# Kernel optimization log

Measured on AMD Instinct MI355X. Metric: run time of the kernel, lower is better.

## Reference

```python
import jax, jax.numpy as jnp
import numpy as np
import math

IN_DIM = 512
OUT_DIM = 512
KEY_DIM = 512
N_HEADS = 8
HEAD_DIM = KEY_DIM // N_HEADS
B, S = 2, 2048


def setup_inputs() -> dict:
    key = jax.random.key(0)
    ks = jax.random.split(key, 9)
    sc = 0.02
    return {
        "x": jax.random.normal(ks[0], (B, IN_DIM, S), dtype=jnp.float32),
        "wq": jax.random.normal(ks[1], (KEY_DIM, IN_DIM), dtype=jnp.float32) * sc,
        "bq": jax.random.normal(ks[2], (KEY_DIM,), dtype=jnp.float32) * sc,
        "wk": jax.random.normal(ks[3], (KEY_DIM, IN_DIM), dtype=jnp.float32) * sc,
        "bk": jax.random.normal(ks[4], (KEY_DIM,), dtype=jnp.float32) * sc,
        "wv": jax.random.normal(ks[5], (OUT_DIM, IN_DIM), dtype=jnp.float32) * sc,
        "bv": jax.random.normal(ks[6], (OUT_DIM,), dtype=jnp.float32) * sc,
        "wo": jax.random.normal(ks[7], (OUT_DIM, OUT_DIM), dtype=jnp.float32) * sc,
        "bo": jax.random.normal(ks[8], (OUT_DIM,), dtype=jnp.float32) * sc,
    }


def reference(x, wq, bq, wk, bk, wv, bv, wo, bo):
    # x: (B, C, S). Conv1d with kernel_size=1 == channelwise linear.
    b, _, s = x.shape
    vd = OUT_DIM // N_HEADS  # per-head value dim
    # projections: (B, key_dim, S) -> (B, H, hd, S)
    q = (jnp.einsum('oc,bcs->bos', wq, x) + bq[None, :, None]).reshape(b, N_HEADS, HEAD_DIM, s)
    k = (jnp.einsum('oc,bcs->bos', wk, x) + bk[None, :, None]).reshape(b, N_HEADS, HEAD_DIM, s)
    v = (jnp.einsum('oc,bcs->bos', wv, x) + bv[None, :, None]).reshape(b, N_HEADS, vd, s)
    # scores: (B, H, S, S) = q^T k / sqrt(hd)
    scores = jnp.einsum('bhdt,bhds->bhts', q, k) / math.sqrt(HEAD_DIM)
    attn = jax.nn.softmax(scores, axis=-1)
    # out: (B, H, S_query, vd) -> (B, out_dim, S)
    out = jnp.einsum('bhts,bhds->bhtd', attn, v)
    out = out.transpose(0, 1, 3, 2).reshape(b, OUT_DIM, s)
    out = jnp.einsum('oc,bcs->bos', wo, out) + bo[None, :, None]
    return out
```

## Files before the change

kernel.cpp:

```cpp
#include <hip/hip_runtime.h>
#include <hip/hip_bf16.h>


typedef __attribute__((ext_vector_type(8))) short short8;
typedef __attribute__((ext_vector_type(4))) short short4v;
typedef __attribute__((ext_vector_type(4))) float f32x4;
typedef __attribute__((ext_vector_type(2))) int int2v;

#define DEV static __device__ __forceinline__

DEV short f2bf(float f) {
  union { float f; unsigned u; } v; v.f = f;
  unsigned r = (v.u + 0x7FFFu + ((v.u >> 16) & 1u)) >> 16;
  return (short)r;
}

DEV float bf2f(short s) {
  union { unsigned u; float f; } v;
  v.u = ((unsigned)(unsigned short)s) << 16;
  return v.f;
}

DEV unsigned pk_bf16(float lo, float hi) {
  union { __hip_bfloat162 h; unsigned u; } cv;
  cv.h = __float22bfloat162_rn(float2{lo, hi});
  return cv.u;
}

DEV void gload_lds16(const void* g, void* l) {
  __builtin_amdgcn_global_load_lds((const __attribute__((address_space(1))) void*)g,
                                   (__attribute__((address_space(3))) void*)l, 16, 0, 0);
}

__global__ __launch_bounds__(256) void xpose_k(const float* __restrict__ x, short* __restrict__ xt) {
  __shared__ float tile[32][33];
  const int b = blockIdx.z;
  const int s0 = blockIdx.x * 32, c0 = blockIdx.y * 32;
  const int tl = threadIdx.x & 31, tr = threadIdx.x >> 5;
  const float* src = x + ((size_t)b * 512 + c0) * 2048 + s0;
#pragma unroll
  for (int i = 0; i < 4; ++i)
    tile[tr + i * 8][tl] = src[(size_t)(tr + i * 8) * 2048 + tl];
  __syncthreads();
  short* dst = xt + ((size_t)b * 2048 + s0) * 512 + c0;
#pragma unroll
  for (int i = 0; i < 4; ++i) {
    const int s = tr + i * 8;
    dst[(size_t)s * 512 + tl] = f2bf(tile[tl][s]);
  }
}

__global__ __launch_bounds__(256) void wconv_k(const float* __restrict__ wq, const float* __restrict__ wk,
                                               const float* __restrict__ wv, const float* __restrict__ wo,
                                               short* __restrict__ dst) {
  const int idx = blockIdx.x * 256 + threadIdx.x;
  const int m = idx >> 16;
  const int base = (idx & 65535) * 4;
  const float* src = (m == 0) ? wq : (m == 1) ? wk : (m == 2) ? wv : wo;
  const f32x4 v = *(const f32x4*)(src + base);
  short4v o;
#pragma unroll
  for (int r = 0; r < 4; ++r) o[r] = f2bf(v[r]);
  *(short4v*)(dst + (size_t)idx * 4) = o;
}

template <int MODE>
__global__ __launch_bounds__(256) void gemm_bt_k(const short* __restrict__ A, const short* __restrict__ B,
                                                 void* __restrict__ out, short* __restrict__ out2,
                                                 const float* __restrict__ bias0,
                                                 const float* __restrict__ bias1,
                                                 const float* __restrict__ bias2) {
  constexpr int TM = (MODE == 0) ? 128 : 64;
  constexpr int MI = TM / 32;
  constexpr int ABLK = TM / 32;
  constexpr int NI = (MODE == 0) ? 12 : 64;
  constexpr int CHUNK = (MODE == 0) ? 48 : 32;
  __shared__ short As[TM * 64];
  __shared__ short Bs[128 * 64];
  const int bx0 = blockIdx.x;
  const int bx = (bx0 & 7) * CHUNK + (bx0 >> 3);
  const int it = bx % NI, jt = bx / NI;
  const int tid = threadIdx.x;
  const int lane = tid & 63, wid = tid >> 6;
  const int wi = wid & 1, wj = wid >> 1;
  const int g = lane >> 4, c = lane & 15;

  f32x4 acc[MI][4] = {};

  for (int k0 = 0; k0 < 512; k0 += 64) {
#pragma unroll
    for (int q = 0; q < ABLK; ++q) {
      const int blk = wid * ABLK + q;
      const int row = blk * 8 + (lane >> 3);
      const int ks = ((lane & 7) ^ (row & 7)) * 8;
      gload_lds16(A + (size_t)(it * TM + row) * 512 + k0 + ks, As + blk * 512);
    }
#pragma unroll
    for (int q = 0; q < 4; ++q) {
      const int blk = wid * 4 + q;
      const int row = blk * 8 + (lane >> 3);
      const int ks = ((lane & 7) ^ (row & 7)) * 8;
      gload_lds16(B + (size_t)(jt * 128 + row) * 512 + k0 + ks, Bs + blk * 512);
    }
    __syncthreads();
#pragma unroll
    for (int kk = 0; kk < 2; ++kk) {
      short8 af[MI], bfv[4];
#pragma unroll
      for (int mi = 0; mi < MI; ++mi) {
        const int row = wi * (TM / 2) + mi * 16 + c;
        af[mi] = *(const short8*)(As + ((row * 64 + kk * 32 + g * 8) ^ ((row & 7) << 3)));
      }
#pragma unroll
      for (int nj = 0; nj < 4; ++nj) {
        const int row = wj * 64 + nj * 16 + c;
        bfv[nj] = *(const short8*)(Bs + ((row * 64 + kk * 32 + g * 8) ^ ((row & 7) << 3)));
      }
#pragma unroll
      for (int mi = 0; mi < MI; ++mi)
#pragma unroll
        for (int nj = 0; nj < 4; ++nj)
          acc[mi][nj] = __builtin_amdgcn_mfma_f32_16x16x32_bf16(af[mi], bfv[nj], acc[mi][nj], 0, 0, 0);
    }
    __syncthreads();
  }

  if constexpr (MODE == 0) {
    short* ob = (short*)out;
#pragma unroll
    for (int mi = 0; mi < MI; ++mi) {
      const int i0 = it * 128 + wi * 64 + mi * 16 + g * 4;
      if (i0 < 1024) {
        const bool isQ = i0 < 512;
        const float scale = isQ ? 0.125f : 1.0f;
        const float* bp = isQ ? bias0 : bias1;
        const int boff = isQ ? 0 : 512;
        float b4[4];
#pragma unroll
        for (int r = 0; r < 4; ++r) b4[r] = bp[i0 + r - boff];
#pragma unroll
        for (int nj = 0; nj < 4; ++nj) {
          const int j = jt * 128 + wj * 64 + nj * 16 + c;
          short4v st;
#pragma unroll
          for (int r = 0; r < 4; ++r) st[r] = f2bf((acc[mi][nj][r] + b4[r]) * scale);
          *(short4v*)(ob + (size_t)j * 1024 + i0) = st;
        }
      } else {
        float b4[4];
#pragma unroll
        for (int r = 0; r < 4; ++r) b4[r] = bias2[i0 + r - 1024];
#pragma unroll
        for (int nj = 0; nj < 4; ++nj) {
          const int j = jt * 128 + wj * 64 + nj * 16 + c;
#pragma unroll
          for (int r = 0; r < 4; ++r)
            out2[(size_t)(i0 + r - 1024) * 4096 + j] = f2bf(acc[mi][nj][r] + b4[r]);
        }
      }
    }
  } else {
    float* ob = (float*)out;
#pragma unroll
    for (int mi = 0; mi < MI; ++mi) {
      const int i0 = it * 64 + wi * 32 + mi * 16 + g * 4;
      const int bb = i0 >> 11, t = i0 & 2047;
#pragma unroll
      for (int nj = 0; nj < 4; ++nj) {
        const int j = jt * 128 + wj * 64 + nj * 16 + c;
        const float bj = bias0[j];
        f32x4 st;
#pragma unroll
        for (int r = 0; r < 4; ++r) st[r] = acc[mi][nj][r] + bj;
        *(f32x4*)(ob + ((size_t)(bb * 512 + j)) * 2048 + t) = st;
      }
    }
  }
}

__global__ __launch_bounds__(256, 4) void attn_k(const short* __restrict__ qk, const short* __restrict__ v,
                                                 short* __restrict__ OPB, float* __restrict__ Lb) {
  __shared__ short ks2[2][64 * 64];
  __shared__ short vs2[2][64 * 64];
  __shared__ short pbuf[4][32 * 64];
  const int bid = blockIdx.x;
  const int swz = (bid & 7) * 128 + (bid >> 3);
  const int qt = swz & 15;
  const int grp = swz >> 4;
  const int bh = grp & 15, seg = grp >> 4;
  const int b = bh >> 3, h = bh & 7;
  const int lane = threadIdx.x & 63, wid = threadIdx.x >> 6;
  const int g = lane >> 4, c = lane & 15;
  const int q0 = qt * 128 + wid * 32;
  short* pl = pbuf[wid];

  const short* qp = qk + (size_t)(b * 2048 + q0) * 1024 + h * 64;
  const short* kb = qk + (size_t)(b * 2048) * 1024 + 512 + h * 64;
  const short* vb = v + (size_t)(h * 64) * 4096 + b * 2048;

  short8 qf[2][2];
#pragma unroll
  for (int nj = 0; nj < 2; ++nj)
#pragma unroll
    for (int kk = 0; kk < 2; ++kk)
      qf[nj][kk] = *(const short8*)(qp + (size_t)(nj * 16 + c) * 1024 + kk * 32 + g * 8);

  const int sr = lane >> 3;
  const int scol = ((lane & 7) ^ sr) * 8;

  const int kvbeg = seg * 512;
#pragma unroll
  for (int q = 0; q < 2; ++q) {
    const int blk = wid * 2 + q;
    const int row = blk * 8 + sr;
    gload_lds16(kb + (size_t)(kvbeg + row) * 1024 + scol, &ks2[0][blk * 512]);
    gload_lds16(vb + (size_t)row * 4096 + kvbeg + scol, &vs2[0][blk * 512]);
  }

  f32x4 oacc[4][2] = {};
  float lpart[2] = {0.f, 0.f};
  const float LOG2E = 1.44269504088896f;
  const float M2 = 5.770780163555852f;

  for (int it8 = 0; it8 < 8; ++it8) {
    const int bufi = it8 & 1;

    {
      const int kvn = kvbeg + ((it8 + 1) & 7) * 64;
#pragma unroll
      for (int q = 0; q < 2; ++q) {
        const int blk = wid * 2 + q;
        const int row = blk * 8 + sr;
        gload_lds16(kb + (size_t)(kvn + row) * 1024 + scol, &ks2[bufi ^ 1][blk * 512]);
        gload_lds16(vb + (size_t)row * 4096 + kvn + scol, &vs2[bufi ^ 1][blk * 512]);
      }
    }

    asm volatile("s_waitcnt vmcnt(4)" ::: "memory");
    __builtin_amdgcn_s_barrier();

    f32x4 st[4][2] = {};
    __builtin_amdgcn_s_setprio(1);
#pragma unroll
    for (int kk = 0; kk < 2; ++kk) {
      short8 kf[4];
#pragma unroll
      for (int mi = 0; mi < 4; ++mi) {
        const int row = mi * 16 + c;
        kf[mi] = *(const short8*)(&ks2[bufi][(row * 64 + kk * 32 + g * 8) ^ ((row & 7) << 3)]);
      }
#pragma unroll
      for (int mi = 0; mi < 4; ++mi)
#pragma unroll
        for (int nj = 0; nj < 2; ++nj)
          st[mi][nj] = __builtin_amdgcn_mfma_f32_16x16x32_bf16(kf[mi], qf[nj][kk], st[mi][nj], 0, 0, 0);
    }
    __builtin_amdgcn_s_setprio(0);

#pragma unroll
    for (int mi = 0; mi < 4; ++mi)
#pragma unroll
      for (int nj = 0; nj < 2; ++nj) {
        const float p0 = __builtin_amdgcn_exp2f(__builtin_fmaf(st[mi][nj][0], LOG2E, -M2));
        const float p1 = __builtin_amdgcn_exp2f(__builtin_fmaf(st[mi][nj][1], LOG2E, -M2));
        const float p2 = __builtin_amdgcn_exp2f(__builtin_fmaf(st[mi][nj][2], LOG2E, -M2));
        const float p3 = __builtin_amdgcn_exp2f(__builtin_fmaf(st[mi][nj][3], LOG2E, -M2));
        lpart[nj] += (p0 + p1) + (p2 + p3);
        const unsigned w0 = pk_bf16(p0, p1);
        const unsigned w1 = pk_bf16(p2, p3);
        const int t = nj * 16 + c;
        *(int2v*)(pl + ((t * 64 + mi * 16 + g * 4) ^ ((t & 7) << 3))) = (int2v){(int)w0, (int)w1};
      }

    __builtin_amdgcn_s_setprio(1);
#pragma unroll
    for (int kk = 0; kk < 2; ++kk) {
      short8 vf[4], pa[2];
#pragma unroll
      for (int dj = 0; dj < 4; ++dj) {
        const int row = dj * 16 + c;
        vf[dj] = *(const short8*)(&vs2[bufi][(row * 64 + kk * 32 + g * 8) ^ ((row & 7) << 3)]);
      }
#pragma unroll
      for (int o = 0; o < 2; ++o) {
        const int row = o * 16 + c;
        pa[o] = *(const short8*)(pl + ((row * 64 + kk * 32 + g * 8) ^ ((row & 7) << 3)));
      }
#pragma unroll
      for (int dj = 0; dj < 4; ++dj)
#pragma unroll
        for (int o = 0; o < 2; ++o)
          oacc[dj][o] = __builtin_amdgcn_mfma_f32_16x16x32_bf16(vf[dj], pa[o], oacc[dj][o], 0, 0, 0);
    }
    __builtin_amdgcn_s_setprio(0);

    asm volatile("s_waitcnt lgkmcnt(0)" ::: "memory");
    __builtin_amdgcn_s_barrier();
  }

  float lrow[2];
#pragma unroll
  for (int nj = 0; nj < 2; ++nj) {
    float a = lpart[nj];
    a += __shfl_xor(a, 16);
    a += __shfl_xor(a, 32);
    lrow[nj] = a;
  }
  const size_t rbase = (size_t)seg * 32768 + (size_t)bh * 2048 + q0;
#pragma unroll
  for (int o = 0; o < 2; ++o) {
    const int t = o * 16 + c;
#pragma unroll
    for (int dj = 0; dj < 4; ++dj) {
      short4v w;
#pragma unroll
      for (int r = 0; r < 4; ++r) w[r] = f2bf(oacc[dj][o][r]);
      *(short4v*)(OPB + (rbase + t) * 64 + dj * 16 + g * 4) = w;
    }
    if (g == 0) Lb[rbase + t] = lrow[o];
  }
  asm volatile("s_waitcnt vmcnt(0)" ::: "memory");
}

__global__ __launch_bounds__(256) void merge_k(const short* __restrict__ OPB, const float* __restrict__ Lb,
                                               short* __restrict__ o) {
  const int gid = blockIdx.x * 256 + threadIdx.x;
  const int row = gid >> 2;
  const int dg = (gid & 3) * 16;
  float L = 0.f;
#pragma unroll
  for (int s = 0; s < 4; ++s) L += Lb[s * 32768 + row];
  const float rinv = 1.f / L;
  float acc[16];
#pragma unroll
  for (int j = 0; j < 16; ++j) acc[j] = 0.f;
#pragma unroll
  for (int s = 0; s < 4; ++s) {
#pragma unroll
    for (int q = 0; q < 2; ++q) {
      const short8 vv = *(const short8*)(OPB + ((size_t)s * 32768 + row) * 64 + dg + q * 8);
#pragma unroll
      for (int r = 0; r < 8; ++r) acc[q * 8 + r] += bf2f(vv[r]);
    }
  }
  const int bh = row >> 11, srow = row & 2047;
  const int b = bh >> 3, h = bh & 7;
  short8 st[2];
#pragma unroll
  for (int j = 0; j < 16; ++j) st[j >> 3][j & 7] = f2bf(acc[j] * rinv);
  short* dst = o + (size_t)(b * 2048 + srow) * 512 + h * 64 + dg;
  *(short8*)dst = st[0];
  *(short8*)(dst + 8) = st[1];
}

extern "C" void kernel_launch(void* const* d_in, const int* in_sizes, int n_in,
                              void* d_out, int out_size, void* d_ws, size_t ws_size,
                              hipStream_t stream) {
  const float* x  = (const float*)d_in[0];
  const float* wq = (const float*)d_in[1];
  const float* bq = (const float*)d_in[2];
  const float* wk = (const float*)d_in[3];
  const float* bk = (const float*)d_in[4];
  const float* wv = (const float*)d_in[5];
  const float* bv = (const float*)d_in[6];
  const float* wo = (const float*)d_in[7];
  const float* bo = (const float*)d_in[8];

  short* XT  = (short*)d_ws;
  short* WQKV = XT + (size_t)4096 * 512;
  short* WO  = WQKV + (size_t)1536 * 512;
  short* QKB = WO + (size_t)512 * 512;
  short* VB  = QKB + (size_t)4096 * 1024;
  short* OB  = VB + (size_t)512 * 4096;
  short* OPB = OB + (size_t)4096 * 512;
  float* Lb  = (float*)(OPB + (size_t)4 * 32768 * 64);

  xpose_k<<<dim3(64, 16, 2), 256, 0, stream>>>(x, XT);
  wconv_k<<<dim3(1024), 256, 0, stream>>>(wq, wk, wv, wo, WQKV);
  gemm_bt_k<0><<<dim3(384), 256, 0, stream>>>(WQKV, XT, (void*)QKB, VB, bq, bk, bv);
  attn_k<<<dim3(1024), 256, 0, stream>>>(QKB, VB, OPB, Lb);
  merge_k<<<dim3(512), 256, 0, stream>>>(OPB, Lb, OB);
  gemm_bt_k<2><<<dim3(256), 256, 0, stream>>>(OB, WO, d_out, nullptr, bo, nullptr, nullptr);
}
```

Baseline: 75.45 us.

## Fuse split-KV merge into output projection GEMM and merge prep kernels

Folds the split-KV merge (summing four partial outputs and normalising by the summed row sums) into the A-tile load of the output projection GEMM, so the normalised attention output is written straight to shared memory instead of round-tripping through a global buffer. It also combines the transpose and weight-conversion kernels into one launch and specialises the GEMM template to its QKV mode. In the attention loop it moves the barrier to the top of each iteration with a full vmcnt(0) wait before issuing the next prefetch, dropping the end-of-iteration lgkm wait and barrier. This removes two launches and an intermediate buffer, but the output GEMM now redoes the merge work once per column tile (four times in total), and the attention loop's prefetch overlap changes.

```diff
diff --git a/kernel.cpp b/kernel.cpp
--- a/kernel.cpp
+++ b/kernel.cpp
@@ -6,6 +6,7 @@
 typedef __attribute__((ext_vector_type(4))) short short4v;
 typedef __attribute__((ext_vector_type(4))) float f32x4;
 typedef __attribute__((ext_vector_type(2))) int int2v;
+typedef __attribute__((ext_vector_type(4))) int int4v;
 
 #define DEV static __device__ __forceinline__
 
@@ -32,36 +33,38 @@
                                    (__attribute__((address_space(3))) void*)l, 16, 0, 0);
 }
 
-__global__ __launch_bounds__(256) void xpose_k(const float* __restrict__ x, short* __restrict__ xt) {
+__global__ __launch_bounds__(256) void prep_k(const float* __restrict__ x, short* __restrict__ xt,
+                                              const float* __restrict__ wq, const float* __restrict__ wk,
+                                              const float* __restrict__ wv, const float* __restrict__ wo,
+                                              short* __restrict__ wdst) {
   __shared__ float tile[32][33];
-  const int b = blockIdx.z;
-  const int s0 = blockIdx.x * 32, c0 = blockIdx.y * 32;
-  const int tl = threadIdx.x & 31, tr = threadIdx.x >> 5;
-  const float* src = x + ((size_t)b * 512 + c0) * 2048 + s0;
-#pragma unroll
-  for (int i = 0; i < 4; ++i)
-    tile[tr + i * 8][tl] = src[(size_t)(tr + i * 8) * 2048 + tl];
-  __syncthreads();
-  short* dst = xt + ((size_t)b * 2048 + s0) * 512 + c0;
-#pragma unroll
-  for (int i = 0; i < 4; ++i) {
-    const int s = tr + i * 8;
-    dst[(size_t)s * 512 + tl] = f2bf(tile[tl][s]);
-  }
-}
-
-__global__ __launch_bounds__(256) void wconv_k(const float* __restrict__ wq, const float* __restrict__ wk,
-                                               const float* __restrict__ wv, const float* __restrict__ wo,
-                                               short* __restrict__ dst) {
-  const int idx = blockIdx.x * 256 + threadIdx.x;
-  const int m = idx >> 16;
-  const int base = (idx & 65535) * 4;
-  const float* src = (m == 0) ? wq : (m == 1) ? wk : (m == 2) ? wv : wo;
-  const f32x4 v = *(const f32x4*)(src + base);
-  short4v o;
-#pragma unroll
-  for (int r = 0; r < 4; ++r) o[r] = f2bf(v[r]);
-  *(short4v*)(dst + (size_t)idx * 4) = o;
+  const int bid = blockIdx.x;
+  if (bid < 2048) {
+    const int b = bid >> 10, rest = bid & 1023;
+    const int s0 = (rest & 63) * 32, c0 = (rest >> 6) * 32;
+    const int tl = threadIdx.x & 31, tr = threadIdx.x >> 5;
+    const float* src = x + ((size_t)b * 512 + c0) * 2048 + s0;
+#pragma unroll
+    for (int i = 0; i < 4; ++i)
+      tile[tr + i * 8][tl] = src[(size_t)(tr + i * 8) * 2048 + tl];
+    __syncthreads();
+    short* dst = xt + ((size_t)b * 2048 + s0) * 512 + c0;
+#pragma unroll
+    for (int i = 0; i < 4; ++i) {
+      const int s = tr + i * 8;
+      dst[(size_t)s * 512 + tl] = f2bf(tile[tl][s]);
+    }
+  } else {
+    const int idx = (bid - 2048) * 256 + threadIdx.x;
+    const int m = idx >> 16;
+    const int base = (idx & 65535) * 4;
+    const float* src = (m == 0) ? wq : (m == 1) ? wk : (m == 2) ? wv : wo;
+    const f32x4 v = *(const f32x4*)(src + base);
+    short4v o;
+#pragma unroll
+    for (int r = 0; r < 4; ++r) o[r] = f2bf(v[r]);
+    *(short4v*)(wdst + (size_t)idx * 4) = o;
+  }
 }
 
 template <int MODE>
@@ -70,12 +73,9 @@
                                                  const float* __restrict__ bias0,
                                                  const float* __restrict__ bias1,
                                                  const float* __restrict__ bias2) {
-  constexpr int TM = (MODE == 0) ? 128 : 64;
-  constexpr int MI = TM / 32;
-  constexpr int ABLK = TM / 32;
-  constexpr int NI = (MODE == 0) ? 12 : 64;
-  constexpr int CHUNK = (MODE == 0) ? 48 : 32;
-  __shared__ short As[TM * 64];
+  constexpr int NI = 12;
+  constexpr int CHUNK = 48;
+  __shared__ short As[128 * 64];
   __shared__ short Bs[128 * 64];
   const int bx0 = blockIdx.x;
   const int bx = (bx0 & 7) * CHUNK + (bx0 >> 3);
@@ -85,30 +85,24 @@
   const int wi = wid & 1, wj = wid >> 1;
   const int g = lane >> 4, c = lane & 15;
 
-  f32x4 acc[MI][4] = {};
+  f32x4 acc[4][4] = {};
 
   for (int k0 = 0; k0 < 512; k0 += 64) {
-#pragma unroll
-    for (int q = 0; q < ABLK; ++q) {
-      const int blk = wid * ABLK + q;
-      const int row = blk * 8 + (lane >> 3);
-      const int ks = ((lane & 7) ^ (row & 7)) * 8;
-      gload_lds16(A + (size_t)(it * TM + row) * 512 + k0 + ks, As + blk * 512);
-    }
 #pragma unroll
     for (int q = 0; q < 4; ++q) {
       const int blk = wid * 4 + q;
       const int row = blk * 8 + (lane >> 3);
       const int ks = ((lane & 7) ^ (row & 7)) * 8;
+      gload_lds16(A + (size_t)(it * 128 + row) * 512 + k0 + ks, As + blk * 512);
       gload_lds16(B + (size_t)(jt * 128 + row) * 512 + k0 + ks, Bs + blk * 512);
     }
     __syncthreads();
 #pragma unroll
     for (int kk = 0; kk < 2; ++kk) {
-      short8 af[MI], bfv[4];
-#pragma unroll
-      for (int mi = 0; mi < MI; ++mi) {
-        const int row = wi * (TM / 2) + mi * 16 + c;
+      short8 af[4], bfv[4];
+#pragma unroll
+      for (int mi = 0; mi < 4; ++mi) {
+        const int row = wi * 64 + mi * 16 + c;
         af[mi] = *(const short8*)(As + ((row * 64 + kk * 32 + g * 8) ^ ((row & 7) << 3)));
       }
 #pragma unroll
@@ -117,7 +111,7 @@
         bfv[nj] = *(const short8*)(Bs + ((row * 64 + kk * 32 + g * 8) ^ ((row & 7) << 3)));
       }
 #pragma unroll
-      for (int mi = 0; mi < MI; ++mi)
+      for (int mi = 0; mi < 4; ++mi)
 #pragma unroll
         for (int nj = 0; nj < 4; ++nj)
           acc[mi][nj] = __builtin_amdgcn_mfma_f32_16x16x32_bf16(af[mi], bfv[nj], acc[mi][nj], 0, 0, 0);
@@ -125,54 +119,36 @@
     __syncthreads();
   }
 
-  if constexpr (MODE == 0) {
-    short* ob = (short*)out;
-#pragma unroll
-    for (int mi = 0; mi < MI; ++mi) {
-      const int i0 = it * 128 + wi * 64 + mi * 16 + g * 4;
-      if (i0 < 1024) {
-        const bool isQ = i0 < 512;
-        const float scale = isQ ? 0.125f : 1.0f;
-        const float* bp = isQ ? bias0 : bias1;
-        const int boff = isQ ? 0 : 512;
-        float b4[4];
-#pragma unroll
-        for (int r = 0; r < 4; ++r) b4[r] = bp[i0 + r - boff];
-#pragma unroll
-        for (int nj = 0; nj < 4; ++nj) {
-          const int j = jt * 128 + wj * 64 + nj * 16 + c;
-          short4v st;
-#pragma unroll
-          for (int r = 0; r < 4; ++r) st[r] = f2bf((acc[mi][nj][r] + b4[r]) * scale);
-          *(short4v*)(ob + (size_t)j * 1024 + i0) = st;
-        }
-      } else {
-        float b4[4];
-#pragma unroll
-        for (int r = 0; r < 4; ++r) b4[r] = bias2[i0 + r - 1024];
-#pragma unroll
-        for (int nj = 0; nj < 4; ++nj) {
-          const int j = jt * 128 + wj * 64 + nj * 16 + c;
-#pragma unroll
-          for (int r = 0; r < 4; ++r)
-            out2[(size_t)(i0 + r - 1024) * 4096 + j] = f2bf(acc[mi][nj][r] + b4[r]);
-        }
-      }
-    }
-  } else {
-    float* ob = (float*)out;
-#pragma unroll
-    for (int mi = 0; mi < MI; ++mi) {
-      const int i0 = it * 64 + wi * 32 + mi * 16 + g * 4;
-      const int bb = i0 >> 11, t = i0 & 2047;
+  short* ob = (short*)out;
+#pragma unroll
+  for (int mi = 0; mi < 4; ++mi) {
+    const int i0 = it * 128 + wi * 64 + mi * 16 + g * 4;
+    if (i0 < 1024) {
+      const bool isQ = i0 < 512;
+      const float scale = isQ ? 0.125f : 1.0f;
+      const float* bp = isQ ? bias0 : bias1;
+      const int boff = isQ ? 0 : 512;
+      float b4[4];
+#pragma unroll
+      for (int r = 0; r < 4; ++r) b4[r] = bp[i0 + r - boff];
 #pragma unroll
       for (int nj = 0; nj < 4; ++nj) {
         const int j = jt * 128 + wj * 64 + nj * 16 + c;
-        const float bj = bias0[j];
-        f32x4 st;
-#pragma unroll
-        for (int r = 0; r < 4; ++r) st[r] = acc[mi][nj][r] + bj;
-        *(f32x4*)(ob + ((size_t)(bb * 512 + j)) * 2048 + t) = st;
+        short4v st;
+#pragma unroll
+        for (int r = 0; r < 4; ++r) st[r] = f2bf((acc[mi][nj][r] + b4[r]) * scale);
+        *(short4v*)(ob + (size_t)j * 1024 + i0) = st;
+      }
+    } else {
+      float b4[4];
+#pragma unroll
+      for (int r = 0; r < 4; ++r) b4[r] = bias2[i0 + r - 1024];
+#pragma unroll
+      for (int nj = 0; nj < 4; ++nj) {
+        const int j = jt * 128 + wj * 64 + nj * 16 + c;
+#pragma unroll
+        for (int r = 0; r < 4; ++r)
+          out2[(size_t)(i0 + r - 1024) * 4096 + j] = f2bf(acc[mi][nj][r] + b4[r]);
       }
     }
   }
@@ -225,6 +201,9 @@
   for (int it8 = 0; it8 < 8; ++it8) {
     const int bufi = it8 & 1;
 
+    asm volatile("s_waitcnt vmcnt(0)" ::: "memory");
+    __builtin_amdgcn_s_barrier();
+
     {
       const int kvn = kvbeg + ((it8 + 1) & 7) * 64;
 #pragma unroll
@@ -235,9 +214,6 @@
         gload_lds16(vb + (size_t)row * 4096 + kvn + scol, &vs2[bufi ^ 1][blk * 512]);
       }
     }
-
-    asm volatile("s_waitcnt vmcnt(4)" ::: "memory");
-    __builtin_amdgcn_s_barrier();
 
     f32x4 st[4][2] = {};
     __builtin_amdgcn_s_setprio(1);
@@ -293,9 +269,6 @@
           oacc[dj][o] = __builtin_amdgcn_mfma_f32_16x16x32_bf16(vf[dj], pa[o], oacc[dj][o], 0, 0, 0);
     }
     __builtin_amdgcn_s_setprio(0);
-
-    asm volatile("s_waitcnt lgkmcnt(0)" ::: "memory");
-    __builtin_amdgcn_s_barrier();
   }
 
   float lrow[2];
@@ -322,35 +295,99 @@
   asm volatile("s_waitcnt vmcnt(0)" ::: "memory");
 }
 
-__global__ __launch_bounds__(256) void merge_k(const short* __restrict__ OPB, const float* __restrict__ Lb,
-                                               short* __restrict__ o) {
-  const int gid = blockIdx.x * 256 + threadIdx.x;
-  const int row = gid >> 2;
-  const int dg = (gid & 3) * 16;
-  float L = 0.f;
-#pragma unroll
-  for (int s = 0; s < 4; ++s) L += Lb[s * 32768 + row];
-  const float rinv = 1.f / L;
-  float acc[16];
-#pragma unroll
-  for (int j = 0; j < 16; ++j) acc[j] = 0.f;
-#pragma unroll
-  for (int s = 0; s < 4; ++s) {
-#pragma unroll
-    for (int q = 0; q < 2; ++q) {
-      const short8 vv = *(const short8*)(OPB + ((size_t)s * 32768 + row) * 64 + dg + q * 8);
-#pragma unroll
-      for (int r = 0; r < 8; ++r) acc[q * 8 + r] += bf2f(vv[r]);
-    }
-  }
-  const int bh = row >> 11, srow = row & 2047;
-  const int b = bh >> 3, h = bh & 7;
-  short8 st[2];
-#pragma unroll
-  for (int j = 0; j < 16; ++j) st[j >> 3][j & 7] = f2bf(acc[j] * rinv);
-  short* dst = o + (size_t)(b * 2048 + srow) * 512 + h * 64 + dg;
-  *(short8*)dst = st[0];
-  *(short8*)(dst + 8) = st[1];
+__global__ __launch_bounds__(256) void gemm_out_k(const short* __restrict__ OPB,
+                                                  const float* __restrict__ Lb,
+                                                  const short* __restrict__ Bw,
+                                                  float* __restrict__ out,
+                                                  const float* __restrict__ bias) {
+  __shared__ short As[64 * 64];
+  __shared__ short Bs[128 * 64];
+  const int bx0 = blockIdx.x;
+  const int bx = (bx0 & 7) * 32 + (bx0 >> 3);
+  const int it = bx & 63, jt = bx >> 6;
+  const int tid = threadIdx.x;
+  const int lane = tid & 63, wid = tid >> 6;
+  const int wi = wid & 1, wj = wid >> 1;
+  const int g = lane >> 4, c = lane & 15;
+  const int bb = it >> 5;
+  const int t0 = (it & 31) * 64;
+  const int ar = tid >> 2;
+  const int adq = (tid & 3) * 16;
+  const int trow = t0 + ar;
+
+  f32x4 acc[2][4] = {};
+
+  for (int ks = 0; ks < 8; ++ks) {
+    const int bh = bb * 8 + ks;
+    {
+      float L = 0.f;
+#pragma unroll
+      for (int s = 0; s < 4; ++s) L += Lb[(size_t)s * 32768 + bh * 2048 + trow];
+      const float rinv = 1.f / L;
+      float a16[16];
+#pragma unroll
+      for (int r = 0; r < 16; ++r) a16[r] = 0.f;
+#pragma unroll
+      for (int s = 0; s < 4; ++s) {
+        const short* src = OPB + ((size_t)s * 32768 + bh * 2048 + trow) * 64 + adq;
+        const short8 v0 = *(const short8*)(src);
+        const short8 v1 = *(const short8*)(src + 8);
+#pragma unroll
+        for (int r = 0; r < 8; ++r) { a16[r] += bf2f(v0[r]); a16[8 + r] += bf2f(v1[r]); }
+      }
+      int4v w0, w1;
+#pragma unroll
+      for (int r = 0; r < 4; ++r) {
+        w0[r] = (int)pk_bf16(a16[2 * r] * rinv, a16[2 * r + 1] * rinv);
+        w1[r] = (int)pk_bf16(a16[8 + 2 * r] * rinv, a16[9 + 2 * r] * rinv);
+      }
+      *(int4v*)(As + ((ar * 64 + adq) ^ ((ar & 7) << 3))) = w0;
+      *(int4v*)(As + ((ar * 64 + adq + 8) ^ ((ar & 7) << 3))) = w1;
+    }
+#pragma unroll
+    for (int q = 0; q < 4; ++q) {
+      const int blk = wid * 4 + q;
+      const int row = blk * 8 + (lane >> 3);
+      const int kcol = ((lane & 7) ^ (row & 7)) * 8;
+      gload_lds16(Bw + (size_t)(jt * 128 + row) * 512 + ks * 64 + kcol, Bs + blk * 512);
+    }
+    __syncthreads();
+#pragma unroll
+    for (int kk = 0; kk < 2; ++kk) {
+      short8 af[2], bfv[4];
+#pragma unroll
+      for (int mi = 0; mi < 2; ++mi) {
+        const int row = wi * 32 + mi * 16 + c;
+        af[mi] = *(const short8*)(As + ((row * 64 + kk * 32 + g * 8) ^ ((row & 7) << 3)));
+      }
+#pragma unroll
+      for (int nj = 0; nj < 4; ++nj) {
+        const int row = wj * 64 + nj * 16 + c;
+        bfv[nj] = *(const short8*)(Bs + ((row * 64 + kk * 32 + g * 8) ^ ((row & 7) << 3)));
+      }
+#pragma unroll
+      for (int mi = 0; mi < 2; ++mi)
+#pragma unroll
+        for (int nj = 0; nj < 4; ++nj)
+          acc[mi][nj] = __builtin_amdgcn_mfma_f32_16x16x32_bf16(af[mi], bfv[nj], acc[mi][nj], 0, 0, 0);
+    }
+    __syncthreads();
+  }
+
+#pragma unroll
+  for (int mi = 0; mi < 2; ++mi) {
+    const int i0 = it * 64 + wi * 32 + mi * 16 + g * 4;
+    const int t = i0 & 2047;
+#pragma unroll
+    for (int nj = 0; nj < 4; ++nj) {
+      const int j = jt * 128 + wj * 64 + nj * 16 + c;
+      const float bj = bias[j];
+      f32x4 stv;
+#pragma unroll
+      for (int r = 0; r < 4; ++r) stv[r] = acc[mi][nj][r] + bj;
+      *(f32x4*)(out + ((size_t)(bb * 512 + j)) * 2048 + t) = stv;
+    }
+  }
 }
 
 extern "C" void kernel_launch(void* const* d_in, const int* in_sizes, int n_in,
@@ -371,14 +408,11 @@
   short* WO  = WQKV + (size_t)1536 * 512;
   short* QKB = WO + (size_t)512 * 512;
   short* VB  = QKB + (size_t)4096 * 1024;
-  short* OB  = VB + (size_t)512 * 4096;
-  short* OPB = OB + (size_t)4096 * 512;
+  short* OPB = VB + (size_t)512 * 4096;
   float* Lb  = (float*)(OPB + (size_t)4 * 32768 * 64);
 
-  xpose_k<<<dim3(64, 16, 2), 256, 0, stream>>>(x, XT);
-  wconv_k<<<dim3(1024), 256, 0, stream>>>(wq, wk, wv, wo, WQKV);
+  prep_k<<<dim3(3072), 256, 0, stream>>>(x, XT, wq, wk, wv, wo, WQKV);
   gemm_bt_k<0><<<dim3(384), 256, 0, stream>>>(WQKV, XT, (void*)QKB, VB, bq, bk, bv);
   attn_k<<<dim3(1024), 256, 0, stream>>>(QKB, VB, OPB, Lb);
-  merge_k<<<dim3(512), 256, 0, stream>>>(OPB, Lb, OB);
-  gemm_bt_k<2><<<dim3(256), 256, 0, stream>>>(OB, WO, d_out, nullptr, bo, nullptr, nullptr);
-}
+  gemm_out_k<<<dim3(256), 256, 0, stream>>>(OPB, Lb, WO, (float*)d_out, bo);
+}
```

New measurement: 85.10 us. 1.13x slower.
